# Optimization experiments

Hardware: AMD Instinct MI355X
Metric: run time of the kernel (lower is better)

Reference implementation:

```python
import jax, jax.numpy as jnp
import numpy as np

B, S, D, H = 4, 2048, 1024, 16
DK = D // H


def setup_inputs() -> dict:
    key = jax.random.key(0)
    ks = jax.random.split(key, 12)
    std = 0.02
    inp = {
        "q": jax.random.normal(ks[0], (B, S, D), jnp.float32),
        "k": jax.random.normal(ks[1], (B, S, D), jnp.float32),
        "v": jax.random.normal(ks[2], (B, S, D), jnp.float32),
        # causal mask: 1 above diagonal (positions to be masked with -inf)
        "mask": jnp.triu(jnp.ones((S, S), jnp.int32), k=1)[None, None, :, :],
        "Wq": jax.random.normal(ks[3], (D, D), jnp.float32) * std,
        "bq": jnp.zeros((D,), jnp.float32),
        "Wk": jax.random.normal(ks[4], (D, D), jnp.float32) * std,
        "bk": jnp.zeros((D,), jnp.float32),
        "Wv": jax.random.normal(ks[5], (D, D), jnp.float32) * std,
        "bv": jnp.zeros((D,), jnp.float32),
        "Wo": jax.random.normal(ks[6], (D, D), jnp.float32) * std,
        "bo": jnp.zeros((D,), jnp.float32),
    }
    return inp


def _split_heads(x):
    b, s, d = x.shape
    return x.reshape(b, s, H, DK).transpose(0, 2, 1, 3)  # [B,H,S,DK]


def reference(q, k, v, mask, Wq, bq, Wk, bk, Wv, bv, Wo, bo):
    # linear projections (torch Linear: x @ W.T + b)
    qh = _split_heads(q @ Wq.T + bq)
    kh = _split_heads(k @ Wk.T + bk)
    vh = _split_heads(v @ Wv.T + bv)
    scale = 1.0 / jnp.sqrt(jnp.asarray(DK, qh.dtype))
    scores = jnp.einsum("bhqd,bhkd->bhqk", qh, kh) * scale
    scores = jnp.where(mask == 1, -jnp.inf, scores)
    attn = jax.nn.softmax(scores, axis=-1)
    # dropout is identity in eval mode (deterministic reference)
    out = jnp.einsum("bhqk,bhkd->bhqd", attn, vh)
    concat = out.transpose(0, 2, 1, 3).reshape(q.shape[0], -1, D)
    return concat @ Wo.T + bo
```

## Files before the change

kernel.cpp:

```cpp
#include <hip/hip_runtime.h>
#include <hip/hip_bf16.h>

#define BB  4
#define SS  2048
#define DD  1024
#define HH  16
#define DKK 64

typedef unsigned short u16;
typedef short v8s __attribute__((ext_vector_type(8)));
typedef short v4s __attribute__((ext_vector_type(4)));
typedef float v4f __attribute__((ext_vector_type(4)));
typedef float v16f __attribute__((ext_vector_type(16)));
typedef unsigned int v4u __attribute__((ext_vector_type(4)));

#define MFMA32(a, b, c) __builtin_amdgcn_mfma_f32_32x32x16_bf16(a, b, c, 0, 0, 0)

__device__ __forceinline__ u16 f2b(float x) {
  unsigned int u = __float_as_uint(x);
  unsigned int r = (u + 0x7fffu + ((u >> 16) & 1u)) >> 16;
  return (u16)r;
}

__device__ __forceinline__ unsigned int pkhalf(float a, float b) {
  return __builtin_amdgcn_perm(__float_as_uint(a), __float_as_uint(b), 0x03020706u);
}

__device__ __forceinline__ void gload16(const u16* g, u16* l) {
  __builtin_amdgcn_global_load_lds(
      (const __attribute__((address_space(1))) void*)g,
      (__attribute__((address_space(3))) void*)l, 16, 0, 0);
}

__global__ void cvt_f32_bf16(const float* __restrict__ in, u16* __restrict__ out, int n8) {
  int i = blockIdx.x * blockDim.x + threadIdx.x;
  if (i >= n8) return;
  const float4* p = (const float4*)in + (size_t)i * 2;
  float4 a = p[0], b = p[1];
  v8s r = {(short)f2b(a.x), (short)f2b(a.y), (short)f2b(a.z), (short)f2b(a.w),
           (short)f2b(b.x), (short)f2b(b.y), (short)f2b(b.z), (short)f2b(b.w)};
  *(v8s*)(out + (size_t)i * 8) = r;
}

__global__ void transpose_v(const u16* __restrict__ Vp, u16* __restrict__ VT) {
  __shared__ u16 t[32][33];
  int s0 = blockIdx.x * 32, d0 = blockIdx.y * 32;
  int bh = blockIdx.z, b = bh >> 4, h = bh & 15;
  int j = threadIdx.x & 31, i0 = threadIdx.x >> 5;
#pragma unroll
  for (int rr = 0; rr < 4; ++rr) {
    int i = i0 + rr * 8;
    t[i][j] = Vp[(size_t)(b * SS + s0 + i) * DD + h * DKK + d0 + j];
  }
  __syncthreads();
#pragma unroll
  for (int rr = 0; rr < 4; ++rr) {
    int dd = i0 + rr * 8;
    VT[((size_t)(b * HH + h) * DKK + d0 + dd) * SS + s0 + j] = t[j][dd];
  }
}

template <int OUT_F32>
__global__ __launch_bounds__(256) void gemm_bt2(
    const u16* __restrict__ A, const u16* __restrict__ Bw,
    const float* __restrict__ bias, void* __restrict__ Cp,
    int Nn, int Kk, float oscale) {
  __shared__ u16 As[128][32];
  __shared__ u16 Bs[128][32];
  const int tid = threadIdx.x;
  const int lane = tid & 63, wid = tid >> 6;
  const int wm = wid >> 1, wn = wid & 1;
  const int lr = lane & 15, lg = lane >> 4;
  const int row0 = blockIdx.y * 128, col0 = blockIdx.x * 128;

  v4f zero = {0.f, 0.f, 0.f, 0.f};
  v4f acc[4][4];
#pragma unroll
  for (int m = 0; m < 4; ++m)
#pragma unroll
    for (int n = 0; n < 4; ++n) acc[m][n] = zero;

  const int e0 = 2 * wid * 64 + lane;
  const int e1 = e0 + 64;
  const u16* gA0 = A + (size_t)(row0 + (e0 >> 2)) * Kk + (e0 & 3) * 8;
  const u16* gA1 = A + (size_t)(row0 + (e1 >> 2)) * Kk + (e1 & 3) * 8;
  const u16* gB0 = Bw + (size_t)(col0 + (e0 >> 2)) * Kk + (e0 & 3) * 8;
  const u16* gB1 = Bw + (size_t)(col0 + (e1 >> 2)) * Kk + (e1 & 3) * 8;
  u16* lA0 = &As[0][0] + (2 * wid + 0) * 512;
  u16* lA1 = &As[0][0] + (2 * wid + 1) * 512;
  u16* lB0 = &Bs[0][0] + (2 * wid + 0) * 512;
  u16* lB1 = &Bs[0][0] + (2 * wid + 1) * 512;

  for (int k0 = 0; k0 < Kk; k0 += 32) {
    __syncthreads();
    gload16(gA0 + k0, lA0);
    gload16(gA1 + k0, lA1);
    gload16(gB0 + k0, lB0);
    gload16(gB1 + k0, lB1);
    __syncthreads();

    v8s af[4], bf[4];
#pragma unroll
    for (int m = 0; m < 4; ++m) af[m] = *(const v8s*)&As[wm * 64 + m * 16 + lr][lg * 8];
#pragma unroll
    for (int n = 0; n < 4; ++n) bf[n] = *(const v8s*)&Bs[wn * 64 + n * 16 + lr][lg * 8];
#pragma unroll
    for (int m = 0; m < 4; ++m)
#pragma unroll
      for (int n = 0; n < 4; ++n)
        acc[m][n] = __builtin_amdgcn_mfma_f32_16x16x32_bf16(af[m], bf[n], acc[m][n], 0, 0, 0);
  }

#pragma unroll
  for (int n = 0; n < 4; ++n) {
    int gc = col0 + wn * 64 + n * 16 + lr;
    float bv = bias[gc];
#pragma unroll
    for (int m = 0; m < 4; ++m) {
      int gr0 = row0 + wm * 64 + m * 16 + lg * 4;
#pragma unroll
      for (int r = 0; r < 4; ++r) {
        float v = (acc[m][n][r] + bv) * oscale;
        if constexpr (OUT_F32)
          ((float*)Cp)[(size_t)(gr0 + r) * Nn + gc] = v;
        else
          ((u16*)Cp)[(size_t)(gr0 + r) * Nn + gc] = f2b(v);
      }
    }
  }
}

__device__ __forceinline__ void build_pa(const v16f& p, int hi, v8s& a0, v8s& a1) {
  unsigned int u0 = pkhalf(p[0], p[1]);
  unsigned int u1 = pkhalf(p[2], p[3]);
  unsigned int u2 = pkhalf(p[4], p[5]);
  unsigned int u3 = pkhalf(p[6], p[7]);
  unsigned int u4 = pkhalf(p[8], p[9]);
  unsigned int u5 = pkhalf(p[10], p[11]);
  unsigned int u6 = pkhalf(p[12], p[13]);
  unsigned int u7 = pkhalf(p[14], p[15]);
  unsigned int s0 = hi ? u0 : u2;
  unsigned int s1 = hi ? u1 : u3;
  unsigned int s2 = hi ? u4 : u6;
  unsigned int s3 = hi ? u5 : u7;
  unsigned int r0 = __shfl_xor(s0, 32);
  unsigned int r1 = __shfl_xor(s1, 32);
  unsigned int r2 = __shfl_xor(s2, 32);
  unsigned int r3 = __shfl_xor(s3, 32);
  v4u f0 = {hi ? r0 : u0, hi ? r1 : u1, hi ? u2 : r0, hi ? u3 : r1};
  v4u f1 = {hi ? r2 : u4, hi ? r3 : u5, hi ? u6 : r2, hi ? u7 : r3};
  a0 = __builtin_bit_cast(v8s, f0);
  a1 = __builtin_bit_cast(v8s, f1);
}

__global__ __launch_bounds__(256) void attn_fwd3(
    const u16* __restrict__ Qp, const u16* __restrict__ Kp,
    const u16* __restrict__ VT, u16* __restrict__ O) {
  __shared__ u16 Ks[64][72];
  __shared__ u16 Vs[64][72];
  const int tid = threadIdx.x;
  const int w = tid >> 6, lane = tid & 63;
  const int ql = lane & 31;
  const int hi = lane >> 5;
  const int bh = blockIdx.x, b = bh >> 4, h = bh & 15;
  const int qt = (int)gridDim.y - 1 - (int)blockIdx.y;
  const int q0 = qt * 128;
  const int qw0 = q0 + w * 32;
  const int qg = qw0 + ql;

  v8s qf[4];
  const u16* qbase = Qp + (size_t)(b * SS + qg) * DD + h * DKK + hi * 8;
#pragma unroll
  for (int ks = 0; ks < 4; ++ks) qf[ks] = *(const v8s*)(qbase + ks * 16);

  const int sr = tid >> 3;
  const int sc = (tid & 7) * 8;
  const u16* gK = Kp + (size_t)(b * SS + sr) * DD + h * DKK + sc;
  const u16* gV = VT + ((size_t)bh * DKK + sr) * SS + sc;

  const int nt = 2 * (qt + 1);
  v8s stK0 = *(const v8s*)gK;
  v8s stK1 = *(const v8s*)(gK + (size_t)32 * DD);
  v8s stV0 = *(const v8s*)gV;
  v8s stV1 = *(const v8s*)(gV + (size_t)32 * SS);

  float m2 = -1e30f, l = 0.f;
  v16f o0 = {0, 0, 0, 0, 0, 0, 0, 0, 0, 0, 0, 0, 0, 0, 0, 0};
  v16f o1 = o0;

  for (int t = 0; t < nt; ++t) {
    __syncthreads();
    *(v8s*)&Ks[sr][sc] = stK0;
    *(v8s*)&Ks[sr + 32][sc] = stK1;
    *(v8s*)&Vs[sr][sc] = stV0;
    *(v8s*)&Vs[sr + 32][sc] = stV1;
    if (t + 1 < nt) {
      const u16* nK = gK + (size_t)(t + 1) * 64 * DD;
      const u16* nV = gV + (t + 1) * 64;
      stK0 = *(const v8s*)nK;
      stK1 = *(const v8s*)(nK + (size_t)32 * DD);
      stV0 = *(const v8s*)nV;
      stV1 = *(const v8s*)(nV + (size_t)32 * SS);
    }
    __syncthreads();
    const int kv0 = t * 64;
    if (kv0 > qw0 + 31) continue;

    v16f p0 = {0, 0, 0, 0, 0, 0, 0, 0, 0, 0, 0, 0, 0, 0, 0, 0};
    v16f p1 = p0;
#pragma unroll
    for (int ks = 0; ks < 4; ++ks) {
      v8s a0 = *(const v8s*)&Ks[ql][ks * 16 + hi * 8];
      p0 = MFMA32(a0, qf[ks], p0);
      v8s a1 = *(const v8s*)&Ks[32 + ql][ks * 16 + hi * 8];
      p1 = MFMA32(a1, qf[ks], p1);
    }

    if (kv0 + 63 > qw0) {
#pragma unroll
      for (int r = 0; r < 16; ++r) {
        int row = (r & 3) + 8 * (r >> 2) + 4 * hi;
        if (kv0 + row > qg) p0[r] = -3.0e38f;
        if (kv0 + 32 + row > qg) p1[r] = -3.0e38f;
      }
    }

    float pmax = -3.0e38f;
#pragma unroll
    for (int r = 0; r < 16; ++r) pmax = fmaxf(pmax, fmaxf(p0[r], p1[r]));
    pmax = fmaxf(pmax, __shfl_xor(pmax, 32));

    if (!__all(pmax <= m2 + 11.5f)) {
      float mn = fmaxf(m2, pmax);
      float cf = exp2f(m2 - mn);
      m2 = mn;
      l *= cf;
#pragma unroll
      for (int r = 0; r < 16; ++r) {
        int row = (r & 3) + 8 * (r >> 2) + 4 * hi;
        float cfr = __shfl(cf, row);
        o0[r] *= cfr;
        o1[r] *= cfr;
      }
    }

    float rs = 0.f;
#pragma unroll
    for (int r = 0; r < 16; ++r) {
      p0[r] = exp2f(p0[r] - m2);
      rs += p0[r];
    }
#pragma unroll
    for (int r = 0; r < 16; ++r) {
      p1[r] = exp2f(p1[r] - m2);
      rs += p1[r];
    }
    rs += __shfl_xor(rs, 32);
    l += rs;

    v8s pa00, pa01, pa10, pa11;
    build_pa(p0, hi, pa00, pa01);
    build_pa(p1, hi, pa10, pa11);

    __builtin_amdgcn_s_setprio(1);
    v8s b00 = *(const v8s*)&Vs[ql][hi * 8];
    o0 = MFMA32(pa00, b00, o0);
    v8s b01 = *(const v8s*)&Vs[ql][16 + hi * 8];
    o0 = MFMA32(pa01, b01, o0);
    v8s b02 = *(const v8s*)&Vs[ql][32 + hi * 8];
    o0 = MFMA32(pa10, b02, o0);
    v8s b03 = *(const v8s*)&Vs[ql][48 + hi * 8];
    o0 = MFMA32(pa11, b03, o0);

    v8s b10 = *(const v8s*)&Vs[32 + ql][hi * 8];
    o1 = MFMA32(pa00, b10, o1);
    v8s b11 = *(const v8s*)&Vs[32 + ql][16 + hi * 8];
    o1 = MFMA32(pa01, b11, o1);
    v8s b12 = *(const v8s*)&Vs[32 + ql][32 + hi * 8];
    o1 = MFMA32(pa10, b12, o1);
    v8s b13 = *(const v8s*)&Vs[32 + ql][48 + hi * 8];
    o1 = MFMA32(pa11, b13, o1);
    __builtin_amdgcn_s_setprio(0);
  }

  float linv = 1.f / l;
#pragma unroll
  for (int r = 0; r < 16; ++r) {
    int row = (r & 3) + 8 * (r >> 2) + 4 * hi;
    float lr = __shfl(linv, row);
    size_t obase = (size_t)(b * SS + qw0 + row) * DD + h * DKK + ql;
    O[obase] = f2b(o0[r] * lr);
    O[obase + 32] = f2b(o1[r] * lr);
  }
}

extern "C" void kernel_launch(void* const* d_in, const int* in_sizes, int n_in,
                              void* d_out, int out_size, void* d_ws, size_t ws_size,
                              hipStream_t stream) {
  (void)in_sizes; (void)n_in; (void)out_size; (void)ws_size;
  const float* q  = (const float*)d_in[0];
  const float* k  = (const float*)d_in[1];
  const float* v  = (const float*)d_in[2];
  const float* Wq = (const float*)d_in[4];
  const float* bq = (const float*)d_in[5];
  const float* Wk = (const float*)d_in[6];
  const float* bk = (const float*)d_in[7];
  const float* Wv = (const float*)d_in[8];
  const float* bv = (const float*)d_in[9];
  const float* Wo = (const float*)d_in[10];
  const float* bo = (const float*)d_in[11];

  u16* base = (u16*)d_ws;
  const size_t WE = (size_t)DD * DD;
  const size_t PE = (size_t)BB * SS * DD;
  u16* Wq_b = base;
  u16* Wk_b = Wq_b + WE;
  u16* Wv_b = Wk_b + WE;
  u16* Wo_b = Wv_b + WE;
  u16* Qp = Wo_b + WE;
  u16* Kp = Qp + PE;
  u16* Vp = Kp + PE;
  u16* VT = Vp + PE;
  u16* Op = Vp;

  u16* X0 = (u16*)d_out;
  u16* X1 = X0 + PE;

  cvt_f32_bf16<<<512, 256, 0, stream>>>(Wq, Wq_b, (int)(WE / 8));
  cvt_f32_bf16<<<512, 256, 0, stream>>>(Wk, Wk_b, (int)(WE / 8));
  cvt_f32_bf16<<<512, 256, 0, stream>>>(Wv, Wv_b, (int)(WE / 8));
  cvt_f32_bf16<<<512, 256, 0, stream>>>(Wo, Wo_b, (int)(WE / 8));

  dim3 gg(DD / 128, (BB * SS) / 128);
  const float qsc = 0.125f * 1.44269504f;

  cvt_f32_bf16<<<4096, 256, 0, stream>>>(q, X0, (int)(PE / 8));
  cvt_f32_bf16<<<4096, 256, 0, stream>>>(k, X1, (int)(PE / 8));
  gemm_bt2<0><<<gg, 256, 0, stream>>>(X0, Wq_b, bq, Qp, DD, DD, qsc);
  gemm_bt2<0><<<gg, 256, 0, stream>>>(X1, Wk_b, bk, Kp, DD, DD, 1.0f);
  cvt_f32_bf16<<<4096, 256, 0, stream>>>(v, X0, (int)(PE / 8));
  gemm_bt2<0><<<gg, 256, 0, stream>>>(X0, Wv_b, bv, Vp, DD, DD, 1.0f);

  transpose_v<<<dim3(SS / 32, DKK / 32, BB * HH), 256, 0, stream>>>(Vp, VT);
  attn_fwd3<<<dim3(BB * HH, SS / 128), 256, 0, stream>>>(Qp, Kp, VT, Op);
  gemm_bt2<1><<<gg, 256, 0, stream>>>(Op, Wo_b, bo, d_out, DD, DD, 1.0f);
}
```

Baseline: 255.8 us.

## Batch QKV projections, fuse V transpose into GEMM epilogue, and reorder attention tiles

Merges the four weight conversions and three activation conversions into two batched kernels. The three QKV projections now run as a single 3D-grid GEMM launch. The V projection writes its output directly in transposed layout, which removes the separate transpose kernel and its round-trip through memory. The attention grid becomes 1D, with a fixed permutation of query tiles so that causal blocks of different lengths are spread across waves for better load balance. The risk is that the transposed V store is strided and scattered.

```diff
diff --git a/kernel.cpp b/kernel.cpp
--- a/kernel.cpp
+++ b/kernel.cpp
@@ -32,46 +32,56 @@
       (__attribute__((address_space(3))) void*)l, 16, 0, 0);
 }
 
-__global__ void cvt_f32_bf16(const float* __restrict__ in, u16* __restrict__ out, int n8) {
-  int i = blockIdx.x * blockDim.x + threadIdx.x;
-  if (i >= n8) return;
-  const float4* p = (const float4*)in + (size_t)i * 2;
+__device__ __forceinline__ void cvt8(const float* in, u16* out, size_t j) {
+  const float4* p = (const float4*)(in + j * 8);
   float4 a = p[0], b = p[1];
   v8s r = {(short)f2b(a.x), (short)f2b(a.y), (short)f2b(a.z), (short)f2b(a.w),
            (short)f2b(b.x), (short)f2b(b.y), (short)f2b(b.z), (short)f2b(b.w)};
-  *(v8s*)(out + (size_t)i * 8) = r;
-}
-
-__global__ void transpose_v(const u16* __restrict__ Vp, u16* __restrict__ VT) {
-  __shared__ u16 t[32][33];
-  int s0 = blockIdx.x * 32, d0 = blockIdx.y * 32;
-  int bh = blockIdx.z, b = bh >> 4, h = bh & 15;
-  int j = threadIdx.x & 31, i0 = threadIdx.x >> 5;
-#pragma unroll
-  for (int rr = 0; rr < 4; ++rr) {
-    int i = i0 + rr * 8;
-    t[i][j] = Vp[(size_t)(b * SS + s0 + i) * DD + h * DKK + d0 + j];
-  }
-  __syncthreads();
-#pragma unroll
-  for (int rr = 0; rr < 4; ++rr) {
-    int dd = i0 + rr * 8;
-    VT[((size_t)(b * HH + h) * DKK + d0 + dd) * SS + s0 + j] = t[j][dd];
-  }
-}
-
-template <int OUT_F32>
-__global__ __launch_bounds__(256) void gemm_bt2(
-    const u16* __restrict__ A, const u16* __restrict__ Bw,
-    const float* __restrict__ bias, void* __restrict__ Cp,
-    int Nn, int Kk, float oscale) {
+  *(v8s*)(out + j * 8) = r;
+}
+
+__global__ void cvt3(const float* __restrict__ q, const float* __restrict__ k,
+                     const float* __restrict__ v, u16* __restrict__ x0,
+                     u16* __restrict__ x1, u16* __restrict__ x2) {
+  int i = blockIdx.x * blockDim.x + threadIdx.x;
+  int which = i >> 20;
+  size_t j = (size_t)(i & 0xFFFFF);
+  const float* s = which == 0 ? q : (which == 1 ? k : v);
+  u16* d = which == 0 ? x0 : (which == 1 ? x1 : x2);
+  cvt8(s, d, j);
+}
+
+__global__ void cvtW(const float* __restrict__ a, const float* __restrict__ b,
+                     const float* __restrict__ c, const float* __restrict__ d,
+                     u16* __restrict__ oa, u16* __restrict__ ob,
+                     u16* __restrict__ oc, u16* __restrict__ od) {
+  int i = blockIdx.x * blockDim.x + threadIdx.x;
+  int which = i >> 17;
+  size_t j = (size_t)(i & 0x1FFFF);
+  const float* s = which == 0 ? a : (which == 1 ? b : (which == 2 ? c : d));
+  u16* o = which == 0 ? oa : (which == 1 ? ob : (which == 2 ? oc : od));
+  cvt8(s, o, j);
+}
+
+__global__ __launch_bounds__(256) void gemm_qkv(
+    const u16* __restrict__ X0, const u16* __restrict__ X1, const u16* __restrict__ X2,
+    const u16* __restrict__ Wqb, const u16* __restrict__ Wkb, const u16* __restrict__ Wvb,
+    const float* __restrict__ bq, const float* __restrict__ bk, const float* __restrict__ bv,
+    u16* __restrict__ Qp, u16* __restrict__ Kp, u16* __restrict__ VT, float qsc) {
   __shared__ u16 As[128][32];
   __shared__ u16 Bs[128][32];
+  const int z = blockIdx.z;
+  const u16* A = z == 0 ? X0 : (z == 1 ? X1 : X2);
+  const u16* Bw = z == 0 ? Wqb : (z == 1 ? Wkb : Wvb);
+  const float* bias = z == 0 ? bq : (z == 1 ? bk : bv);
+  const float oscale = z == 0 ? qsc : 1.0f;
+
   const int tid = threadIdx.x;
   const int lane = tid & 63, wid = tid >> 6;
   const int wm = wid >> 1, wn = wid & 1;
   const int lr = lane & 15, lg = lane >> 4;
   const int row0 = blockIdx.y * 128, col0 = blockIdx.x * 128;
+  const int Kk = DD, Nn = DD;
 
   v4f zero = {0.f, 0.f, 0.f, 0.f};
   v4f acc[4][4];
@@ -111,21 +121,99 @@
         acc[m][n] = __builtin_amdgcn_mfma_f32_16x16x32_bf16(af[m], bf[n], acc[m][n], 0, 0, 0);
   }
 
+  if (z < 2) {
+    u16* C = z == 0 ? Qp : Kp;
+#pragma unroll
+    for (int n = 0; n < 4; ++n) {
+      int gc = col0 + wn * 64 + n * 16 + lr;
+      float bv2 = bias[gc];
+#pragma unroll
+      for (int m = 0; m < 4; ++m) {
+        int gr0 = row0 + wm * 64 + m * 16 + lg * 4;
+#pragma unroll
+        for (int r = 0; r < 4; ++r)
+          C[(size_t)(gr0 + r) * Nn + gc] = f2b((acc[m][n][r] + bv2) * oscale);
+      }
+    }
+  } else {
+#pragma unroll
+    for (int n = 0; n < 4; ++n) {
+      int gc = col0 + wn * 64 + n * 16 + lr;
+      float bv2 = bias[gc];
+      int h = gc >> 6, dk = gc & 63;
+#pragma unroll
+      for (int m = 0; m < 4; ++m) {
+        int gr0 = row0 + wm * 64 + m * 16 + lg * 4;
+        int b = gr0 >> 11;
+        int s = gr0 & 2047;
+        u16* vbase = VT + (((size_t)b * HH + h) * DKK + dk) * SS + s;
+#pragma unroll
+        for (int r = 0; r < 4; ++r) vbase[r] = f2b(acc[m][n][r] + bv2);
+      }
+    }
+  }
+}
+
+__global__ __launch_bounds__(256) void gemm_out(
+    const u16* __restrict__ A, const u16* __restrict__ Bw,
+    const float* __restrict__ bias, float* __restrict__ Cp) {
+  __shared__ u16 As[128][32];
+  __shared__ u16 Bs[128][32];
+  const int tid = threadIdx.x;
+  const int lane = tid & 63, wid = tid >> 6;
+  const int wm = wid >> 1, wn = wid & 1;
+  const int lr = lane & 15, lg = lane >> 4;
+  const int row0 = blockIdx.y * 128, col0 = blockIdx.x * 128;
+  const int Kk = DD, Nn = DD;
+
+  v4f zero = {0.f, 0.f, 0.f, 0.f};
+  v4f acc[4][4];
+#pragma unroll
+  for (int m = 0; m < 4; ++m)
+#pragma unroll
+    for (int n = 0; n < 4; ++n) acc[m][n] = zero;
+
+  const int e0 = 2 * wid * 64 + lane;
+  const int e1 = e0 + 64;
+  const u16* gA0 = A + (size_t)(row0 + (e0 >> 2)) * Kk + (e0 & 3) * 8;
+  const u16* gA1 = A + (size_t)(row0 + (e1 >> 2)) * Kk + (e1 & 3) * 8;
+  const u16* gB0 = Bw + (size_t)(col0 + (e0 >> 2)) * Kk + (e0 & 3) * 8;
+  const u16* gB1 = Bw + (size_t)(col0 + (e1 >> 2)) * Kk + (e1 & 3) * 8;
+  u16* lA0 = &As[0][0] + (2 * wid + 0) * 512;
+  u16* lA1 = &As[0][0] + (2 * wid + 1) * 512;
+  u16* lB0 = &Bs[0][0] + (2 * wid + 0) * 512;
+  u16* lB1 = &Bs[0][0] + (2 * wid + 1) * 512;
+
+  for (int k0 = 0; k0 < Kk; k0 += 32) {
+    __syncthreads();
+    gload16(gA0 + k0, lA0);
+    gload16(gA1 + k0, lA1);
+    gload16(gB0 + k0, lB0);
+    gload16(gB1 + k0, lB1);
+    __syncthreads();
+
+    v8s af[4], bf[4];
+#pragma unroll
+    for (int m = 0; m < 4; ++m) af[m] = *(const v8s*)&As[wm * 64 + m * 16 + lr][lg * 8];
+#pragma unroll
+    for (int n = 0; n < 4; ++n) bf[n] = *(const v8s*)&Bs[wn * 64 + n * 16 + lr][lg * 8];
+#pragma unroll
+    for (int m = 0; m < 4; ++m)
+#pragma unroll
+      for (int n = 0; n < 4; ++n)
+        acc[m][n] = __builtin_amdgcn_mfma_f32_16x16x32_bf16(af[m], bf[n], acc[m][n], 0, 0, 0);
+  }
+
 #pragma unroll
   for (int n = 0; n < 4; ++n) {
     int gc = col0 + wn * 64 + n * 16 + lr;
-    float bv = bias[gc];
+    float bv2 = bias[gc];
 #pragma unroll
     for (int m = 0; m < 4; ++m) {
       int gr0 = row0 + wm * 64 + m * 16 + lg * 4;
 #pragma unroll
-      for (int r = 0; r < 4; ++r) {
-        float v = (acc[m][n][r] + bv) * oscale;
-        if constexpr (OUT_F32)
-          ((float*)Cp)[(size_t)(gr0 + r) * Nn + gc] = v;
-        else
-          ((u16*)Cp)[(size_t)(gr0 + r) * Nn + gc] = f2b(v);
-      }
+      for (int r = 0; r < 4; ++r)
+        Cp[(size_t)(gr0 + r) * Nn + gc] = acc[m][n][r] + bv2;
     }
   }
 }
@@ -153,7 +241,7 @@
   a1 = __builtin_bit_cast(v8s, f1);
 }
 
-__global__ __launch_bounds__(256) void attn_fwd3(
+__global__ __launch_bounds__(256) void attn_fwd4(
     const u16* __restrict__ Qp, const u16* __restrict__ Kp,
     const u16* __restrict__ VT, u16* __restrict__ O) {
   __shared__ u16 Ks[64][72];
@@ -162,8 +250,11 @@
   const int w = tid >> 6, lane = tid & 63;
   const int ql = lane & 31;
   const int hi = lane >> 5;
-  const int bh = blockIdx.x, b = bh >> 4, h = bh & 15;
-  const int qt = (int)gridDim.y - 1 - (int)blockIdx.y;
+  const int i = blockIdx.x;
+  const int dw = i >> 8, sl = i & 255;
+  const int bh = sl & 63, g = sl >> 6;
+  const int qt = (int)((0x3210674598BACDEFull >> (4 * (dw * 4 + g))) & 15);
+  const int b = bh >> 4, h = bh & 15;
   const int q0 = qt * 128;
   const int qw0 = q0 + w * 32;
   const int qg = qw0 + ql;
@@ -287,10 +378,10 @@
 #pragma unroll
   for (int r = 0; r < 16; ++r) {
     int row = (r & 3) + 8 * (r >> 2) + 4 * hi;
-    float lr = __shfl(linv, row);
+    float lr2 = __shfl(linv, row);
     size_t obase = (size_t)(b * SS + qw0 + row) * DD + h * DKK + ql;
-    O[obase] = f2b(o0[r] * lr);
-    O[obase + 32] = f2b(o1[r] * lr);
+    O[obase] = f2b(o0[r] * lr2);
+    O[obase + 32] = f2b(o1[r] * lr2);
   }
 }
 
@@ -319,29 +410,24 @@
   u16* Wo_b = Wv_b + WE;
   u16* Qp = Wo_b + WE;
   u16* Kp = Qp + PE;
-  u16* Vp = Kp + PE;
-  u16* VT = Vp + PE;
-  u16* Op = Vp;
+  u16* X2 = Kp + PE;
+  u16* VT = X2 + PE;
+  u16* Op = X2;
 
   u16* X0 = (u16*)d_out;
   u16* X1 = X0 + PE;
 
-  cvt_f32_bf16<<<512, 256, 0, stream>>>(Wq, Wq_b, (int)(WE / 8));
-  cvt_f32_bf16<<<512, 256, 0, stream>>>(Wk, Wk_b, (int)(WE / 8));
-  cvt_f32_bf16<<<512, 256, 0, stream>>>(Wv, Wv_b, (int)(WE / 8));
-  cvt_f32_bf16<<<512, 256, 0, stream>>>(Wo, Wo_b, (int)(WE / 8));
+  const float qsc = 0.125f * 1.44269504f;
+
+  cvtW<<<2048, 256, 0, stream>>>(Wq, Wk, Wv, Wo, Wq_b, Wk_b, Wv_b, Wo_b);
+  cvt3<<<12288, 256, 0, stream>>>(q, k, v, X0, X1, X2);
+
+  dim3 gq(DD / 128, (BB * SS) / 128, 3);
+  gemm_qkv<<<gq, 256, 0, stream>>>(X0, X1, X2, Wq_b, Wk_b, Wv_b,
+                                   bq, bk, bv, Qp, Kp, VT, qsc);
+
+  attn_fwd4<<<1024, 256, 0, stream>>>(Qp, Kp, VT, Op);
 
   dim3 gg(DD / 128, (BB * SS) / 128);
-  const float qsc = 0.125f * 1.44269504f;
-
-  cvt_f32_bf16<<<4096, 256, 0, stream>>>(q, X0, (int)(PE / 8));
-  cvt_f32_bf16<<<4096, 256, 0, stream>>>(k, X1, (int)(PE / 8));
-  gemm_bt2<0><<<gg, 256, 0, stream>>>(X0, Wq_b, bq, Qp, DD, DD, qsc);
-  gemm_bt2<0><<<gg, 256, 0, stream>>>(X1, Wk_b, bk, Kp, DD, DD, 1.0f);
-  cvt_f32_bf16<<<4096, 256, 0, stream>>>(v, X0, (int)(PE / 8));
-  gemm_bt2<0><<<gg, 256, 0, stream>>>(X0, Wv_b, bv, Vp, DD, DD, 1.0f);
-
-  transpose_v<<<dim3(SS / 32, DKK / 32, BB * HH), 256, 0, stream>>>(Vp, VT);
-  attn_fwd3<<<dim3(BB * HH, SS / 128), 256, 0, stream>>>(Qp, Kp, VT, Op);
-  gemm_bt2<1><<<gg, 256, 0, stream>>>(Op, Wo_b, bo, d_out, DD, DD, 1.0f);
-}
+  gemm_out<<<gg, 256, 0, stream>>>(Op, Wo_b, bo, (float*)d_out);
+}
```

After: 226.6 us. 1.13x faster.
